# Kernel optimization log

Hardware: AMD Instinct MI355X
Metric: run time of the kernel (lower is better)

## Reference

```python
import jax, jax.numpy as jnp
import numpy as np

NB, NR = 100000, 200000            # bridge / road node counts
E_BR, E_RB, E_BB = 1000000, 1000000, 500000  # edges per relation
H = 32                             # hidden_channels


def _sage(h_src, h_dst, src, dst, n_dst, Wl, bl, Wr):
    # PyG SAGEConv: lin_l(mean_{j in N(i)} x_j) + lin_r(x_i); lin_r has no bias
    msg = jnp.take(h_src, src, axis=0)                      # [E, H] gather
    s = jax.ops.segment_sum(msg, dst, num_segments=n_dst)   # [n_dst, H] scatter-add
    cnt = jax.ops.segment_sum(jnp.ones((dst.shape[0],), h_src.dtype), dst, num_segments=n_dst)
    mean = s / jnp.maximum(cnt, 1.0)[:, None]                # mean aggregation
    return mean @ Wl + bl + h_dst @ Wr


def setup_inputs():
    key = jax.random.key(0)
    ks = jax.random.split(key, 24)
    n = lambda i, shape, s=0.1: jax.random.normal(ks[i], shape, jnp.float32) * s
    return {
        "x_bridge": n(0, (NB, 16), 1.0),
        "x_road": n(1, (NR, 8), 1.0),
        "src_br": jax.random.randint(ks[2], (E_BR,), 0, NB),
        "dst_br": jax.random.randint(ks[3], (E_BR,), 0, NR),
        "src_rb": jax.random.randint(ks[4], (E_RB,), 0, NR),
        "dst_rb": jax.random.randint(ks[5], (E_RB,), 0, NB),
        "src_bb": jax.random.randint(ks[6], (E_BB,), 0, NB),
        "dst_bb": jax.random.randint(ks[7], (E_BB,), 0, NB),
        "W_enc_b": n(8, (16, H)), "b_enc_b": n(9, (H,)),
        "W_enc_r": n(10, (8, H)), "b_enc_r": n(11, (H,)),
        "Wl_br": n(12, (H, H)), "bl_br": n(13, (H,)), "Wr_br": n(14, (H, H)),
        "Wl_rb": n(15, (H, H)), "bl_rb": n(16, (H,)), "Wr_rb": n(17, (H, H)),
        "Wl_bb": n(18, (H, H)), "bl_bb": n(19, (H,)), "Wr_bb": n(20, (H, H)),
        "Wo": n(21, (H, 1)), "bo": n(22, (1,)),
    }


def reference(x_bridge, x_road, src_br, dst_br, src_rb, dst_rb, src_bb, dst_bb,
              W_enc_b, b_enc_b, W_enc_r, b_enc_r,
              Wl_br, bl_br, Wr_br, Wl_rb, bl_rb, Wr_rb, Wl_bb, bl_bb, Wr_bb,
              Wo, bo):
    # per-node-type encoder + relu
    h_b = jax.nn.relu(x_bridge @ W_enc_b + b_enc_b)          # [NB, H]
    h_r = jax.nn.relu(x_road @ W_enc_r + b_enc_r)            # [NR, H]
    # HeteroConv(aggr='sum'): 'bridge' receives road->bridge and bridge->bridge.
    # (bridge->road output is dead code w.r.t. the returned bridge head; XLA DCEs it.)
    out_b = (_sage(h_r, h_b, src_rb, dst_rb, NB, Wl_rb, bl_rb, Wr_rb)
             + _sage(h_b, h_b, src_bb, dst_bb, NB, Wl_bb, bl_bb, Wr_bb))
    # relu then output Linear on 'bridge'
    return jax.nn.relu(out_b) @ Wo + bo                       # [NB, 1]
```

## Files before the change

### kernel.cpp

```cpp
#include <hip/hip_runtime.h>
#include <hip/hip_fp16.h>

#define H 32
#define TPB 256
#define TPB_P 256
#define TPB2 256
#define EPT 16
#define SLOTS 128
#define CAP 2048
#define MAXBUCK 2048

__global__ void __launch_bounds__(TPB) encoder_kernel(
        const float* __restrict__ x_b, const float* __restrict__ x_r,
        const float* __restrict__ W_b, const float* __restrict__ b_b,
        const float* __restrict__ W_r, const float* __restrict__ b_r,
        __half* __restrict__ h_b16, __half* __restrict__ h_r16,
        int NB, int NR,
        int* __restrict__ gcurp, int NBUCK) {
    int gid = blockIdx.x * TPB + threadIdx.x;
    if (gid < NBUCK) gcurp[gid * 16] = gid * CAP;

    __shared__ float sWb[16][H];
    __shared__ float sWr8[8][H];
    __shared__ float sbb[H];
    __shared__ float sbr[H];
    int t = threadIdx.x;
    for (int i = t; i < 16 * H; i += TPB) ((float*)sWb)[i] = W_b[i];
    for (int i = t; i < 8 * H; i += TPB) ((float*)sWr8)[i] = W_r[i];
    if (t < H) { sbb[t] = b_b[t]; sbr[t] = b_r[t]; }
    __syncthreads();

    long long node = gid;
    if (node < NB) {
        const float4* px = (const float4*)(x_b + node * 16);
        float acc[H];
        #pragma unroll
        for (int j = 0; j < H; ++j) acc[j] = sbb[j];
        #pragma unroll
        for (int c = 0; c < 4; ++c) {
            float4 q = px[c];
            float xs[4] = {q.x, q.y, q.z, q.w};
            #pragma unroll
            for (int u = 0; u < 4; ++u) {
                int k = c * 4 + u;
                #pragma unroll
                for (int j = 0; j < H; ++j)
                    acc[j] = fmaf(xs[u], sWb[k][j], acc[j]);
            }
        }
        __half2 o[H / 2];
        #pragma unroll
        for (int j2 = 0; j2 < H / 2; ++j2)
            o[j2] = __floats2half2_rn(fmaxf(acc[2 * j2], 0.0f), fmaxf(acc[2 * j2 + 1], 0.0f));
        float4* dst = (float4*)(h_b16 + node * H);
        const float4* src = (const float4*)o;
        dst[0] = src[0]; dst[1] = src[1]; dst[2] = src[2]; dst[3] = src[3];
    } else if (node < (long long)NB + NR) {
        long long m = node - NB;
        const float4* px = (const float4*)(x_r + m * 8);
        float acc[H];
        #pragma unroll
        for (int j = 0; j < H; ++j) acc[j] = sbr[j];
        #pragma unroll
        for (int c = 0; c < 2; ++c) {
            float4 q = px[c];
            float xs[4] = {q.x, q.y, q.z, q.w};
            #pragma unroll
            for (int u = 0; u < 4; ++u) {
                int k = c * 4 + u;
                #pragma unroll
                for (int j = 0; j < H; ++j)
                    acc[j] = fmaf(xs[u], sWr8[k][j], acc[j]);
            }
        }
        __half2 o[H / 2];
        #pragma unroll
        for (int j2 = 0; j2 < H / 2; ++j2)
            o[j2] = __floats2half2_rn(fmaxf(acc[2 * j2], 0.0f), fmaxf(acc[2 * j2 + 1], 0.0f));
        float4* dst = (float4*)(h_r16 + m * H);
        const float4* src = (const float4*)o;
        dst[0] = src[0]; dst[1] = src[1]; dst[2] = src[2]; dst[3] = src[3];
    }
}

__global__ void __launch_bounds__(TPB_P) place_kernel(
        const int* __restrict__ src_rb, const int* __restrict__ dst_rb,
        const int* __restrict__ src_bb, const int* __restrict__ dst_bb,
        int* __restrict__ gcurp, int* __restrict__ bins,
        int E_RB, int E_BB, int NB, int NBUCK) {
    __shared__ int lcnt[MAXBUCK];
    __shared__ int wbase[MAXBUCK];
    int t = threadIdx.x;
    for (int i = t; i < MAXBUCK; i += TPB_P) lcnt[i] = 0;
    __syncthreads();
    long long e0 = (long long)blockIdx.x * (TPB_P * EPT);
    long long EA = (long long)E_RB + E_BB;
    int bk[EPT], loc[EPT], pk[EPT];
    #pragma unroll
    for (int j = 0; j < EPT; ++j) {
        long long e = e0 + j * TPB_P + t;
        bk[j] = -1; loc[j] = 0; pk[j] = 0;
        if (e < EA) {
            int s, d;
            if (e < E_RB) { s = src_rb[e]; d = dst_rb[e]; }
            else          { long long e2 = e - E_RB; s = src_bb[e2]; d = NB + dst_bb[e2]; }
            bk[j] = d >> 7;
            pk[j] = (s << 7) | (d & 127);
            loc[j] = atomicAdd(&lcnt[bk[j]], 1);
        }
    }
    __syncthreads();
    for (int i = t; i < NBUCK; i += TPB_P) {
        int c = lcnt[i];
        wbase[i] = c ? atomicAdd(&gcurp[i * 16], c) : 0;
    }
    __syncthreads();
    #pragma unroll
    for (int j = 0; j < EPT; ++j) {
        if (bk[j] >= 0) {
            int gslot = wbase[bk[j]] + loc[j];
            if (gslot < (bk[j] + 1) * CAP)
                bins[gslot] = pk[j];
        }
    }
}

__global__ void __launch_bounds__(TPB2) buildgather_kernel(
        const __half* __restrict__ h_r16, const __half* __restrict__ h_b16,
        const int* __restrict__ bins, const int* __restrict__ gcurp,
        __half* __restrict__ mean16, int NB, int N2) {
    __shared__ int rawbuf[CAP];
    __shared__ int srcbuf[CAP];
    __shared__ int lcnt[SLOTS];
    __shared__ int lbase[SLOTS];
    __shared__ int lcur[SLOTS];
    __shared__ int tmp[SLOTS];
    int t = threadIdx.x;
    int b = blockIdx.x;
    int start = b * CAP;
    int n = gcurp[b * 16] - start;
    if (n > CAP) n = CAP;

    if (t < SLOTS) lcnt[t] = 0;
    __syncthreads();

    {
        int n4 = n >> 2;
        const int4* bins4 = (const int4*)(bins + start);
        for (int i = t; i < n4; i += TPB2) {
            int4 p = bins4[i];
            ((int4*)rawbuf)[i] = p;
            atomicAdd(&lcnt[p.x & 127], 1);
            atomicAdd(&lcnt[p.y & 127], 1);
            atomicAdd(&lcnt[p.z & 127], 1);
            atomicAdd(&lcnt[p.w & 127], 1);
        }
        for (int i = (n4 << 2) + t; i < n; i += TPB2) {
            int packed = bins[start + i];
            rawbuf[i] = packed;
            atomicAdd(&lcnt[packed & 127], 1);
        }
    }
    __syncthreads();

    if (t < SLOTS) tmp[t] = lcnt[t];
    __syncthreads();
    for (int off = 1; off < SLOTS; off <<= 1) {
        int x = (t >= off && t < SLOTS) ? tmp[t - off] : 0;
        __syncthreads();
        if (t < SLOTS) tmp[t] += x;
        __syncthreads();
    }
    if (t < SLOTS) { lbase[t] = tmp[t] - lcnt[t]; lcur[t] = tmp[t] - lcnt[t]; }
    __syncthreads();

    for (int i = t; i < n; i += TPB2) {
        int packed = rawbuf[i];
        int slot = atomicAdd(&lcur[packed & 127], 1);
        srcbuf[slot] = packed >> 7;
    }
    __syncthreads();

    int lane = t & 15, g = t >> 4;
    long long base_slot = (long long)b << 7;
    for (int sl = g; sl < SLOTS; sl += (TPB2 / 16)) {
        long long gd = base_slot + sl;
        if (gd >= N2) break;
        const __half* __restrict__ hs = (gd < NB) ? h_r16 : h_b16;
        int off = lbase[sl];
        int cnt = lcnt[sl];
        float ax = 0.0f, ay = 0.0f;
        int k = 0;
        for (; k + 8 <= cnt; k += 8) {
            int s[8];
            #pragma unroll
            for (int j = 0; j < 8; ++j) s[j] = srcbuf[off + k + j];
            float2 f[8];
            #pragma unroll
            for (int j = 0; j < 8; ++j)
                f[j] = __half22float2(*(const __half2*)(hs + (long long)s[j] * H + 2 * lane));
            #pragma unroll
            for (int j = 0; j < 8; ++j) { ax += f[j].x; ay += f[j].y; }
        }
        if (k + 4 <= cnt) {
            int s[4];
            #pragma unroll
            for (int j = 0; j < 4; ++j) s[j] = srcbuf[off + k + j];
            float2 f[4];
            #pragma unroll
            for (int j = 0; j < 4; ++j)
                f[j] = __half22float2(*(const __half2*)(hs + (long long)s[j] * H + 2 * lane));
            #pragma unroll
            for (int j = 0; j < 4; ++j) { ax += f[j].x; ay += f[j].y; }
            k += 4;
        }
        for (; k < cnt; ++k) {
            int s = srcbuf[off + k];
            float2 f = __half22float2(*(const __half2*)(hs + (long long)s * H + 2 * lane));
            ax += f.x; ay += f.y;
        }
        float inv = 1.0f / fmaxf((float)cnt, 1.0f);
        *(__half2*)(mean16 + gd * H + 2 * lane) = __floats2half2_rn(ax * inv, ay * inv);
    }
}

__global__ void __launch_bounds__(TPB) head_kernel(
        const __half* __restrict__ h_b16,
        const __half* __restrict__ mean16,
        const float* __restrict__ Wl_rb,
        const float* __restrict__ bl_rb,
        const float* __restrict__ Wl_bb,
        const float* __restrict__ bl_bb,
        const float* __restrict__ Wr_rb,
        const float* __restrict__ Wr_bb,
        const float* __restrict__ Wo,
        const float* __restrict__ bo,
        float* __restrict__ y, int N) {
    __shared__ float sWl_rb[H][H];
    __shared__ float sWl_bb[H][H];
    __shared__ float sWr[H][H];
    __shared__ float sbl[H];
    __shared__ float sWo[H];
    __shared__ float sbo;

    int t = threadIdx.x;
    for (int i = t; i < H * H; i += blockDim.x) {
        ((float*)sWl_rb)[i] = Wl_rb[i];
        ((float*)sWl_bb)[i] = Wl_bb[i];
        ((float*)sWr)[i]    = Wr_rb[i] + Wr_bb[i];
    }
    if (t < H) {
        sbl[t] = bl_rb[t] + bl_bb[t];
        sWo[t] = Wo[t];
    }
    if (t == 0) sbo = bo[0];
    __syncthreads();

    int node = blockIdx.x * TPB + t;
    if (node >= N) return;

    const float4* pr = (const float4*)(mean16 + (long long)node * H);
    const float4* pb = (const float4*)(mean16 + ((long long)N + node) * H);
    const float4* ph = (const float4*)(h_b16 + (long long)node * H);

    float acc[H];
    #pragma unroll
    for (int j = 0; j < H; ++j) acc[j] = sbl[j];

    #pragma unroll
    for (int c = 0; c < 4; ++c) {
        float4 qr = pr[c];
        float4 qb = pb[c];
        float4 qh = ph[c];
        const __half2* hr = (const __half2*)&qr;
        const __half2* hb = (const __half2*)&qb;
        const __half2* hh = (const __half2*)&qh;
        #pragma unroll
        for (int u = 0; u < 4; ++u) {
            float2 fr = __half22float2(hr[u]);
            float2 fb = __half22float2(hb[u]);
            float2 fh = __half22float2(hh[u]);
            int k0 = c * 8 + u * 2;
            #pragma unroll
            for (int j = 0; j < H; ++j) {
                acc[j] = fmaf(fr.x, sWl_rb[k0][j], acc[j]);
                acc[j] = fmaf(fb.x, sWl_bb[k0][j], acc[j]);
                acc[j] = fmaf(fh.x, sWr[k0][j], acc[j]);
                acc[j] = fmaf(fr.y, sWl_rb[k0 + 1][j], acc[j]);
                acc[j] = fmaf(fb.y, sWl_bb[k0 + 1][j], acc[j]);
                acc[j] = fmaf(fh.y, sWr[k0 + 1][j], acc[j]);
            }
        }
    }

    float out = 0.0f;
    #pragma unroll
    for (int j = 0; j < H; ++j)
        out = fmaf(fmaxf(acc[j], 0.0f), sWo[j], out);
    y[node] = out + sbo;
}

extern "C" void kernel_launch(void* const* d_in, const int* in_sizes, int n_in,
                              void* d_out, int out_size, void* d_ws, size_t ws_size,
                              hipStream_t stream) {
    const float* x_bridge = (const float*)d_in[0];
    const float* x_road   = (const float*)d_in[1];
    const int* src_rb = (const int*)d_in[4];
    const int* dst_rb = (const int*)d_in[5];
    const int* src_bb = (const int*)d_in[6];
    const int* dst_bb = (const int*)d_in[7];
    const float* W_enc_b = (const float*)d_in[8];
    const float* b_enc_b = (const float*)d_in[9];
    const float* W_enc_r = (const float*)d_in[10];
    const float* b_enc_r = (const float*)d_in[11];
    const float* Wl_rb = (const float*)d_in[15];
    const float* bl_rb = (const float*)d_in[16];
    const float* Wr_rb = (const float*)d_in[17];
    const float* Wl_bb = (const float*)d_in[18];
    const float* bl_bb = (const float*)d_in[19];
    const float* Wr_bb = (const float*)d_in[20];
    const float* Wo = (const float*)d_in[21];
    const float* bo = (const float*)d_in[22];
    float* y = (float*)d_out;

    const int NB = in_sizes[0] / 16;
    const int NR = in_sizes[1] / 8;
    const int E_RB = in_sizes[4];
    const int E_BB = in_sizes[6];
    const int N2 = 2 * NB;
    const long long E_ALL = (long long)E_RB + E_BB;
    const int NBUCK = (N2 + SLOTS - 1) / SLOTS;

    char* wp = (char*)d_ws;
    __half* h_r16  = (__half*)wp; wp += (size_t)NR * H * sizeof(__half);
    __half* h_b16  = (__half*)wp; wp += (size_t)NB * H * sizeof(__half);
    __half* mean16 = (__half*)wp; wp += (size_t)N2 * H * sizeof(__half);
    int* bins  = (int*)wp;       wp += (size_t)NBUCK * CAP * sizeof(int);
    int* gcurp = (int*)wp;       wp += (size_t)NBUCK * 16 * sizeof(int);

    {
        long long nodes = (long long)NB + NR;
        int blocks = (int)((nodes + TPB - 1) / TPB);
        encoder_kernel<<<blocks, TPB, 0, stream>>>(x_bridge, x_road,
                                                   W_enc_b, b_enc_b, W_enc_r, b_enc_r,
                                                   h_b16, h_r16, NB, NR, gcurp, NBUCK);
    }

    int nWGe = (int)((E_ALL + (TPB_P * EPT) - 1) / (TPB_P * EPT));
    place_kernel<<<nWGe, TPB_P, 0, stream>>>(src_rb, dst_rb, src_bb, dst_bb,
                                             gcurp, bins, E_RB, E_BB, NB, NBUCK);

    buildgather_kernel<<<NBUCK, TPB2, 0, stream>>>(h_r16, h_b16, bins, gcurp,
                                                   mean16, NB, N2);

    head_kernel<<<(NB + TPB - 1) / TPB, TPB, 0, stream>>>(h_b16, mean16,
                                                  Wl_rb, bl_rb, Wl_bb, bl_bb,
                                                  Wr_rb, Wr_bb, Wo, bo, y, NB);
}
```

Measured before the change: 103.5 us.

## Fuse encoder and edge-binning kernels into one launch with memset-initialized cursors

Merges the encoder and edge placement kernels into a single prep kernel, with blocks split by index between node encoding and edge bucketing. This lets the two independent stages run concurrently and saves one launch. The bucket cursors become relative counts zeroed by hipMemsetAsync, which replaces the initialization the encoder used to do and so removes the ordering dependency. The buildgather kernel now reads the count directly. The fused kernel carries the union of both stages' shared memory per block, which may lower occupancy.

```diff
diff --git a/kernel.cpp b/kernel.cpp
--- a/kernel.cpp
+++ b/kernel.cpp
@@ -3,129 +3,123 @@
 
 #define H 32
 #define TPB 256
-#define TPB_P 256
-#define TPB2 256
 #define EPT 16
 #define SLOTS 128
 #define CAP 2048
 #define MAXBUCK 2048
 
-__global__ void __launch_bounds__(TPB) encoder_kernel(
+__global__ void __launch_bounds__(TPB) prep_kernel(
         const float* __restrict__ x_b, const float* __restrict__ x_r,
         const float* __restrict__ W_b, const float* __restrict__ b_b,
         const float* __restrict__ W_r, const float* __restrict__ b_r,
         __half* __restrict__ h_b16, __half* __restrict__ h_r16,
-        int NB, int NR,
-        int* __restrict__ gcurp, int NBUCK) {
-    int gid = blockIdx.x * TPB + threadIdx.x;
-    if (gid < NBUCK) gcurp[gid * 16] = gid * CAP;
-
-    __shared__ float sWb[16][H];
-    __shared__ float sWr8[8][H];
-    __shared__ float sbb[H];
-    __shared__ float sbr[H];
-    int t = threadIdx.x;
-    for (int i = t; i < 16 * H; i += TPB) ((float*)sWb)[i] = W_b[i];
-    for (int i = t; i < 8 * H; i += TPB) ((float*)sWr8)[i] = W_r[i];
-    if (t < H) { sbb[t] = b_b[t]; sbr[t] = b_r[t]; }
-    __syncthreads();
-
-    long long node = gid;
-    if (node < NB) {
-        const float4* px = (const float4*)(x_b + node * 16);
-        float acc[H];
-        #pragma unroll
-        for (int j = 0; j < H; ++j) acc[j] = sbb[j];
-        #pragma unroll
-        for (int c = 0; c < 4; ++c) {
-            float4 q = px[c];
-            float xs[4] = {q.x, q.y, q.z, q.w};
-            #pragma unroll
-            for (int u = 0; u < 4; ++u) {
-                int k = c * 4 + u;
-                #pragma unroll
-                for (int j = 0; j < H; ++j)
-                    acc[j] = fmaf(xs[u], sWb[k][j], acc[j]);
-            }
-        }
-        __half2 o[H / 2];
-        #pragma unroll
-        for (int j2 = 0; j2 < H / 2; ++j2)
-            o[j2] = __floats2half2_rn(fmaxf(acc[2 * j2], 0.0f), fmaxf(acc[2 * j2 + 1], 0.0f));
-        float4* dst = (float4*)(h_b16 + node * H);
-        const float4* src = (const float4*)o;
-        dst[0] = src[0]; dst[1] = src[1]; dst[2] = src[2]; dst[3] = src[3];
-    } else if (node < (long long)NB + NR) {
-        long long m = node - NB;
-        const float4* px = (const float4*)(x_r + m * 8);
-        float acc[H];
-        #pragma unroll
-        for (int j = 0; j < H; ++j) acc[j] = sbr[j];
-        #pragma unroll
-        for (int c = 0; c < 2; ++c) {
-            float4 q = px[c];
-            float xs[4] = {q.x, q.y, q.z, q.w};
-            #pragma unroll
-            for (int u = 0; u < 4; ++u) {
-                int k = c * 4 + u;
-                #pragma unroll
-                for (int j = 0; j < H; ++j)
-                    acc[j] = fmaf(xs[u], sWr8[k][j], acc[j]);
-            }
-        }
-        __half2 o[H / 2];
-        #pragma unroll
-        for (int j2 = 0; j2 < H / 2; ++j2)
-            o[j2] = __floats2half2_rn(fmaxf(acc[2 * j2], 0.0f), fmaxf(acc[2 * j2 + 1], 0.0f));
-        float4* dst = (float4*)(h_r16 + m * H);
-        const float4* src = (const float4*)o;
-        dst[0] = src[0]; dst[1] = src[1]; dst[2] = src[2]; dst[3] = src[3];
-    }
-}
-
-__global__ void __launch_bounds__(TPB_P) place_kernel(
+        int NB, int NR, int encBlocks,
         const int* __restrict__ src_rb, const int* __restrict__ dst_rb,
         const int* __restrict__ src_bb, const int* __restrict__ dst_bb,
         int* __restrict__ gcurp, int* __restrict__ bins,
-        int E_RB, int E_BB, int NB, int NBUCK) {
-    __shared__ int lcnt[MAXBUCK];
-    __shared__ int wbase[MAXBUCK];
+        int E_RB, int E_BB, int NBUCK) {
     int t = threadIdx.x;
-    for (int i = t; i < MAXBUCK; i += TPB_P) lcnt[i] = 0;
-    __syncthreads();
-    long long e0 = (long long)blockIdx.x * (TPB_P * EPT);
-    long long EA = (long long)E_RB + E_BB;
-    int bk[EPT], loc[EPT], pk[EPT];
-    #pragma unroll
-    for (int j = 0; j < EPT; ++j) {
-        long long e = e0 + j * TPB_P + t;
-        bk[j] = -1; loc[j] = 0; pk[j] = 0;
-        if (e < EA) {
-            int s, d;
-            if (e < E_RB) { s = src_rb[e]; d = dst_rb[e]; }
-            else          { long long e2 = e - E_RB; s = src_bb[e2]; d = NB + dst_bb[e2]; }
-            bk[j] = d >> 7;
-            pk[j] = (s << 7) | (d & 127);
-            loc[j] = atomicAdd(&lcnt[bk[j]], 1);
-        }
-    }
-    __syncthreads();
-    for (int i = t; i < NBUCK; i += TPB_P) {
-        int c = lcnt[i];
-        wbase[i] = c ? atomicAdd(&gcurp[i * 16], c) : 0;
-    }
-    __syncthreads();
-    #pragma unroll
-    for (int j = 0; j < EPT; ++j) {
-        if (bk[j] >= 0) {
-            int gslot = wbase[bk[j]] + loc[j];
-            if (gslot < (bk[j] + 1) * CAP)
-                bins[gslot] = pk[j];
+
+    if (blockIdx.x < encBlocks) {
+        __shared__ float sWb[16][H];
+        __shared__ float sWr8[8][H];
+        __shared__ float sbb[H];
+        __shared__ float sbr[H];
+        for (int i = t; i < 16 * H; i += TPB) ((float*)sWb)[i] = W_b[i];
+        for (int i = t; i < 8 * H; i += TPB) ((float*)sWr8)[i] = W_r[i];
+        if (t < H) { sbb[t] = b_b[t]; sbr[t] = b_r[t]; }
+        __syncthreads();
+
+        long long node = (long long)blockIdx.x * TPB + t;
+        if (node < NB) {
+            const float4* px = (const float4*)(x_b + node * 16);
+            float acc[H];
+            #pragma unroll
+            for (int j = 0; j < H; ++j) acc[j] = sbb[j];
+            #pragma unroll
+            for (int c = 0; c < 4; ++c) {
+                float4 q = px[c];
+                float xs[4] = {q.x, q.y, q.z, q.w};
+                #pragma unroll
+                for (int u = 0; u < 4; ++u) {
+                    int k = c * 4 + u;
+                    #pragma unroll
+                    for (int j = 0; j < H; ++j)
+                        acc[j] = fmaf(xs[u], sWb[k][j], acc[j]);
+                }
+            }
+            __half2 o[H / 2];
+            #pragma unroll
+            for (int j2 = 0; j2 < H / 2; ++j2)
+                o[j2] = __floats2half2_rn(fmaxf(acc[2 * j2], 0.0f), fmaxf(acc[2 * j2 + 1], 0.0f));
+            float4* dst = (float4*)(h_b16 + node * H);
+            const float4* src = (const float4*)o;
+            dst[0] = src[0]; dst[1] = src[1]; dst[2] = src[2]; dst[3] = src[3];
+        } else if (node < (long long)NB + NR) {
+            long long m = node - NB;
+            const float4* px = (const float4*)(x_r + m * 8);
+            float acc[H];
+            #pragma unroll
+            for (int j = 0; j < H; ++j) acc[j] = sbr[j];
+            #pragma unroll
+            for (int c = 0; c < 2; ++c) {
+                float4 q = px[c];
+                float xs[4] = {q.x, q.y, q.z, q.w};
+                #pragma unroll
+                for (int u = 0; u < 4; ++u) {
+                    int k = c * 4 + u;
+                    #pragma unroll
+                    for (int j = 0; j < H; ++j)
+                        acc[j] = fmaf(xs[u], sWr8[k][j], acc[j]);
+                }
+            }
+            __half2 o[H / 2];
+            #pragma unroll
+            for (int j2 = 0; j2 < H / 2; ++j2)
+                o[j2] = __floats2half2_rn(fmaxf(acc[2 * j2], 0.0f), fmaxf(acc[2 * j2 + 1], 0.0f));
+            float4* dst = (float4*)(h_r16 + m * H);
+            const float4* src = (const float4*)o;
+            dst[0] = src[0]; dst[1] = src[1]; dst[2] = src[2]; dst[3] = src[3];
+        }
+    } else {
+        __shared__ int lcnt[MAXBUCK];
+        __shared__ int wbase[MAXBUCK];
+        for (int i = t; i < MAXBUCK; i += TPB) lcnt[i] = 0;
+        __syncthreads();
+        long long e0 = (long long)(blockIdx.x - encBlocks) * (TPB * EPT);
+        long long EA = (long long)E_RB + E_BB;
+        int bk[EPT], loc[EPT], pk[EPT];
+        #pragma unroll
+        for (int j = 0; j < EPT; ++j) {
+            long long e = e0 + j * TPB + t;
+            bk[j] = -1; loc[j] = 0; pk[j] = 0;
+            if (e < EA) {
+                int s, d;
+                if (e < E_RB) { s = src_rb[e]; d = dst_rb[e]; }
+                else          { long long e2 = e - E_RB; s = src_bb[e2]; d = NB + dst_bb[e2]; }
+                bk[j] = d >> 7;
+                pk[j] = (s << 7) | (d & 127);
+                loc[j] = atomicAdd(&lcnt[bk[j]], 1);
+            }
+        }
+        __syncthreads();
+        for (int i = t; i < NBUCK; i += TPB) {
+            int c = lcnt[i];
+            wbase[i] = c ? (i * CAP + atomicAdd(&gcurp[i * 16], c)) : 0;
+        }
+        __syncthreads();
+        #pragma unroll
+        for (int j = 0; j < EPT; ++j) {
+            if (bk[j] >= 0) {
+                int gslot = wbase[bk[j]] + loc[j];
+                if (gslot < (bk[j] + 1) * CAP)
+                    bins[gslot] = pk[j];
+            }
         }
     }
 }
 
-__global__ void __launch_bounds__(TPB2) buildgather_kernel(
+__global__ void __launch_bounds__(TPB) buildgather_kernel(
         const __half* __restrict__ h_r16, const __half* __restrict__ h_b16,
         const int* __restrict__ bins, const int* __restrict__ gcurp,
         __half* __restrict__ mean16, int NB, int N2) {
@@ -138,7 +132,7 @@
     int t = threadIdx.x;
     int b = blockIdx.x;
     int start = b * CAP;
-    int n = gcurp[b * 16] - start;
+    int n = gcurp[b * 16];
     if (n > CAP) n = CAP;
 
     if (t < SLOTS) lcnt[t] = 0;
@@ -147,7 +141,7 @@
     {
         int n4 = n >> 2;
         const int4* bins4 = (const int4*)(bins + start);
-        for (int i = t; i < n4; i += TPB2) {
+        for (int i = t; i < n4; i += TPB) {
             int4 p = bins4[i];
             ((int4*)rawbuf)[i] = p;
             atomicAdd(&lcnt[p.x & 127], 1);
@@ -155,7 +149,7 @@
             atomicAdd(&lcnt[p.z & 127], 1);
             atomicAdd(&lcnt[p.w & 127], 1);
         }
-        for (int i = (n4 << 2) + t; i < n; i += TPB2) {
+        for (int i = (n4 << 2) + t; i < n; i += TPB) {
             int packed = bins[start + i];
             rawbuf[i] = packed;
             atomicAdd(&lcnt[packed & 127], 1);
@@ -174,7 +168,7 @@
     if (t < SLOTS) { lbase[t] = tmp[t] - lcnt[t]; lcur[t] = tmp[t] - lcnt[t]; }
     __syncthreads();
 
-    for (int i = t; i < n; i += TPB2) {
+    for (int i = t; i < n; i += TPB) {
         int packed = rawbuf[i];
         int slot = atomicAdd(&lcur[packed & 127], 1);
         srcbuf[slot] = packed >> 7;
@@ -183,7 +177,7 @@
 
     int lane = t & 15, g = t >> 4;
     long long base_slot = (long long)b << 7;
-    for (int sl = g; sl < SLOTS; sl += (TPB2 / 16)) {
+    for (int sl = g; sl < SLOTS; sl += (TPB / 16)) {
         long long gd = base_slot + sl;
         if (gd >= N2) break;
         const __half* __restrict__ hs = (gd < NB) ? h_r16 : h_b16;
@@ -338,20 +332,18 @@
     int* bins  = (int*)wp;       wp += (size_t)NBUCK * CAP * sizeof(int);
     int* gcurp = (int*)wp;       wp += (size_t)NBUCK * 16 * sizeof(int);
 
-    {
-        long long nodes = (long long)NB + NR;
-        int blocks = (int)((nodes + TPB - 1) / TPB);
-        encoder_kernel<<<blocks, TPB, 0, stream>>>(x_bridge, x_road,
-                                                   W_enc_b, b_enc_b, W_enc_r, b_enc_r,
-                                                   h_b16, h_r16, NB, NR, gcurp, NBUCK);
-    }
-
-    int nWGe = (int)((E_ALL + (TPB_P * EPT) - 1) / (TPB_P * EPT));
-    place_kernel<<<nWGe, TPB_P, 0, stream>>>(src_rb, dst_rb, src_bb, dst_bb,
-                                             gcurp, bins, E_RB, E_BB, NB, NBUCK);
-
-    buildgather_kernel<<<NBUCK, TPB2, 0, stream>>>(h_r16, h_b16, bins, gcurp,
-                                                   mean16, NB, N2);
+    hipMemsetAsync(gcurp, 0, (size_t)NBUCK * 16 * sizeof(int), stream);
+
+    long long nodes = (long long)NB + NR;
+    int encBlocks = (int)((nodes + TPB - 1) / TPB);
+    int placeBlocks = (int)((E_ALL + (TPB * EPT) - 1) / (TPB * EPT));
+    prep_kernel<<<encBlocks + placeBlocks, TPB, 0, stream>>>(
+        x_bridge, x_road, W_enc_b, b_enc_b, W_enc_r, b_enc_r,
+        h_b16, h_r16, NB, NR, encBlocks,
+        src_rb, dst_rb, src_bb, dst_bb, gcurp, bins, E_RB, E_BB, NBUCK);
+
+    buildgather_kernel<<<NBUCK, TPB, 0, stream>>>(h_r16, h_b16, bins, gcurp,
+                                                  mean16, NB, N2);
 
     head_kernel<<<(NB + TPB - 1) / TPB, TPB, 0, stream>>>(h_b16, mean16,
                                                   Wl_rb, bl_rb, Wl_bb, bl_bb,
```

Result: faster. 97.02 us (-6.3%).
